# Kernel optimization log

Hardware: AMD Instinct MI355X
Metric: run time of the kernel (lower is better)

## Reference

```python
import jax, jax.numpy as jnp
import numpy as np

N_EMBD = 768
N_HEAD = 12
BLOCK_SIZE = 1024


def setup_inputs() -> dict:
    key = jax.random.key(0)
    ks = jax.random.split(key, 11)
    s = lambda fan_in: 1.0 / np.sqrt(fan_in)
    x = jax.random.normal(ks[0], (8, 1024, N_EMBD), dtype=jnp.float32)
    return {
        "x": x,
        "ln1_g": jnp.ones((N_EMBD,), jnp.float32),
        "ln1_b": jnp.zeros((N_EMBD,), jnp.float32),
        "w_attn": jax.random.normal(ks[1], (N_EMBD, 3 * N_EMBD), jnp.float32) * s(N_EMBD),
        "b_attn": jnp.zeros((3 * N_EMBD,), jnp.float32),
        "w_proj": jax.random.normal(ks[2], (N_EMBD, N_EMBD), jnp.float32) * s(N_EMBD),
        "b_proj": jnp.zeros((N_EMBD,), jnp.float32),
        "ln2_g": jnp.ones((N_EMBD,), jnp.float32),
        "ln2_b": jnp.zeros((N_EMBD,), jnp.float32),
        "w_fc": jax.random.normal(ks[3], (N_EMBD, 4 * N_EMBD), jnp.float32) * s(N_EMBD),
        "b_fc": jnp.zeros((4 * N_EMBD,), jnp.float32),
        "w_fc_proj": jax.random.normal(ks[4], (4 * N_EMBD, N_EMBD), jnp.float32) * s(4 * N_EMBD),
        "b_fc_proj": jnp.zeros((N_EMBD,), jnp.float32),
    }


def _layernorm(x, g, b, eps=1e-5):
    mu = jnp.mean(x, axis=-1, keepdims=True)
    var = jnp.var(x, axis=-1, keepdims=True)
    return (x - mu) * jax.lax.rsqrt(var + eps) * g + b


def _gelu_tanh(x):
    # GELU with tanh approximation (matches nn.GELU(approximate='tanh'))
    c = np.sqrt(2.0 / np.pi).astype(np.float32)
    return 0.5 * x * (1.0 + jnp.tanh(c * (x + 0.044715 * x * x * x)))


def _attn(x, w_attn, b_attn, w_proj, b_proj):
    B, T, C = x.shape
    hs = C // N_HEAD
    qkv = x @ w_attn + b_attn  # [B,T,3C]
    q, k, v = jnp.split(qkv, 3, axis=-1)
    # [B,T,C] -> [B,nh,T,hs]
    to_heads = lambda t: t.reshape(B, T, N_HEAD, hs).transpose(0, 2, 1, 3)
    q, k, v = to_heads(q), to_heads(k), to_heads(v)
    att = jnp.einsum('bhqd,bhkd->bhqk', q, k) * (1.0 / np.sqrt(hs))
    causal = jnp.tril(jnp.ones((T, T), bool))
    att = jnp.where(causal, att, -jnp.inf)
    att = jax.nn.softmax(att, axis=-1)
    y = jnp.einsum('bhqk,bhkd->bhqd', att, v)  # [B,nh,T,hs]
    y = y.transpose(0, 2, 1, 3).reshape(B, T, C)
    return y @ w_proj + b_proj


def reference(x, ln1_g, ln1_b, w_attn, b_attn, w_proj, b_proj,
              ln2_g, ln2_b, w_fc, b_fc, w_fc_proj, b_fc_proj):
    x = x + _attn(_layernorm(x, ln1_g, ln1_b), w_attn, b_attn, w_proj, b_proj)
    h = _layernorm(x, ln2_g, ln2_b)
    h = _gelu_tanh(h @ w_fc + b_fc) @ w_fc_proj + b_fc_proj
    return x + h
```

## Files before the change

kernel.cpp:

```cpp
#include <hip/hip_runtime.h>

typedef __bf16 bf16x8 __attribute__((ext_vector_type(8)));
typedef float  f32x4  __attribute__((ext_vector_type(4)));
typedef unsigned short ushort8 __attribute__((ext_vector_type(8)));

__device__ __forceinline__ unsigned short f2bf(float f) {
    unsigned u = __float_as_uint(f);
    u += 0x7FFFu + ((u >> 16) & 1u);
    return (unsigned short)(u >> 16);
}

__device__ __forceinline__ f32x4 mfma16x16x32(bf16x8 a, bf16x8 b, f32x4 c) {
    return __builtin_amdgcn_mfma_f32_16x16x32_bf16(a, b, c, 0, 0, 0);
}

__device__ __forceinline__ bf16x8 ld8(const unsigned short* p) {
    return __builtin_bit_cast(bf16x8, *(const ushort8*)p);
}

__device__ __forceinline__ float exp2_fast(float x) {
    float r; asm("v_exp_f32 %0, %1" : "=v"(r) : "v"(x)); return r;
}

__device__ __forceinline__ void glds16(const unsigned short* g, unsigned short* l) {
    __builtin_amdgcn_global_load_lds(
        (const __attribute__((address_space(1))) void*)g,
        (__attribute__((address_space(3))) void*)l, 16, 0, 0);
}

__device__ __forceinline__ float gelu_tanh(float x) {
    const float c = 0.7978845608028654f;
    float z = c * (x + 0.044715f * x * x * x);
    float e = __expf(2.f * z);
    float th = 1.f - 2.f / (e + 1.f);
    return 0.5f * x * (1.f + th);
}

#define N_EMBD 768
#define SEQ    1024
#define NHEAD  12
#define HS     64
#define MROWS  8192

__global__ __launch_bounds__(256) void tcast_kernel(const float* __restrict__ in,
                                                    unsigned short* __restrict__ out,
                                                    int K, int N) {
    __shared__ float tile[32][33];
    int nb = blockIdx.x * 32, kb = blockIdx.y * 32;
    int tx = threadIdx.x, ty = threadIdx.y;
#pragma unroll
    for (int i = 0; i < 4; i++) {
        int k = kb + ty + i * 8;
        tile[ty + i * 8][tx] = in[(size_t)k * N + nb + tx];
    }
    __syncthreads();
#pragma unroll
    for (int i = 0; i < 4; i++) {
        int n = nb + ty + i * 8;
        out[(size_t)n * K + kb + tx] = f2bf(tile[tx][ty + i * 8]);
    }
}

__global__ __launch_bounds__(256) void ln_kernel(const float* __restrict__ x,
                                                 const float* __restrict__ g,
                                                 const float* __restrict__ b,
                                                 unsigned short* __restrict__ out) {
    int row = blockIdx.x;
    const float* xr = x + (size_t)row * N_EMBD;
    float v[3], s = 0.f, s2 = 0.f;
#pragma unroll
    for (int i = 0; i < 3; i++) {
        v[i] = xr[threadIdx.x + i * 256];
        s += v[i]; s2 += v[i] * v[i];
    }
#pragma unroll
    for (int m = 1; m < 64; m <<= 1) { s += __shfl_xor(s, m); s2 += __shfl_xor(s2, m); }
    __shared__ float ps[4], ps2[4];
    int wid = threadIdx.x >> 6;
    if ((threadIdx.x & 63) == 0) { ps[wid] = s; ps2[wid] = s2; }
    __syncthreads();
    s  = ps[0] + ps[1] + ps[2] + ps[3];
    s2 = ps2[0] + ps2[1] + ps2[2] + ps2[3];
    float mu  = s * (1.f / N_EMBD);
    float var = s2 * (1.f / N_EMBD) - mu * mu;
    float inv = rsqrtf(var + 1e-5f);
#pragma unroll
    for (int i = 0; i < 3; i++) {
        int c = threadIdx.x + i * 256;
        out[(size_t)row * N_EMBD + c] = f2bf((v[i] - mu) * inv * g[c] + b[c]);
    }
}

template <int EPI, int WM>
__global__ __launch_bounds__(256) void gemm_bt_kernel(
    const unsigned short* __restrict__ A, const unsigned short* __restrict__ BT,
    const float* __restrict__ bias, const float* __restrict__ res,
    float* __restrict__ outF, unsigned short* __restrict__ outB,
    int M, int N, int K) {
    constexpr int BM = WM * 32;
    constexpr int ASZ = BM * 64;
    constexpr int BSZ = 128 * 64;
    __shared__ __attribute__((aligned(16))) unsigned short As[2 * ASZ];
    __shared__ __attribute__((aligned(16))) unsigned short Bs[2 * BSZ];
    const int gx = gridDim.x;
    const int slot = blockIdx.y * gx + blockIdx.x;
    const int chunk = (gx * gridDim.y) >> 3;
    const int logical = (slot & 7) * chunk + (slot >> 3);
    const int m0 = (logical / gx) * BM, n0 = (logical % gx) * 128;
    const int t = threadIdx.x, lane = t & 63, wid = t >> 6;
    const int wr = wid >> 1, wc = wid & 1;

    f32x4 acc[WM][4] = {};

    const int rrow = lane & 15, g = lane >> 4;
    const int swz8 = (rrow & 7) << 3;

    const int srow = t >> 3;
    const int scol = ((t & 7) ^ (srow & 7)) * 8;

    const int NT = K >> 6;
#pragma unroll
    for (int i = 0; i < WM; i++)
        glds16(&A[(size_t)(m0 + i * 32 + srow) * K + scol], &As[i * 2048 + wid * 512]);
#pragma unroll
    for (int i = 0; i < 4; i++)
        glds16(&BT[(size_t)(n0 + i * 32 + srow) * K + scol], &Bs[i * 2048 + wid * 512]);
    __syncthreads();

    int cur = 0;
    for (int kt = 0; kt < NT; ++kt) {
        if (kt + 1 < NT) {
            const int kk = (kt + 1) << 6;
            const int nb = (cur ^ 1);
#pragma unroll
            for (int i = 0; i < WM; i++)
                glds16(&A[(size_t)(m0 + i * 32 + srow) * K + kk + scol],
                       &As[nb * ASZ + i * 2048 + wid * 512]);
#pragma unroll
            for (int i = 0; i < 4; i++)
                glds16(&BT[(size_t)(n0 + i * 32 + srow) * K + kk + scol],
                       &Bs[nb * BSZ + i * 2048 + wid * 512]);
        }
        const unsigned short* ab = &As[cur * ASZ];
        const unsigned short* bb = &Bs[cur * BSZ];
#pragma unroll
        for (int s = 0; s < 2; s++) {
            bf16x8 af[WM], bfr[4];
#pragma unroll
            for (int i = 0; i < WM; i++) {
                int row = wr * (WM * 16) + i * 16 + rrow;
                af[i] = ld8(&ab[row * 64 + ((((s << 2) | g) << 3) ^ swz8)]);
            }
#pragma unroll
            for (int j = 0; j < 4; j++) {
                int row = wc * 64 + j * 16 + rrow;
                bfr[j] = ld8(&bb[row * 64 + ((((s << 2) | g) << 3) ^ swz8)]);
            }
#pragma unroll
            for (int i = 0; i < WM; i++)
#pragma unroll
                for (int j = 0; j < 4; j++) acc[i][j] = mfma16x16x32(af[i], bfr[j], acc[i][j]);
        }
        __syncthreads();
        cur ^= 1;
    }

    const int crow = g * 4, ccol = rrow;
#pragma unroll
    for (int i = 0; i < WM; i++) {
        int gr0 = m0 + wr * (WM * 16) + i * 16 + crow;
#pragma unroll
        for (int j = 0; j < 4; j++) {
            int gc = n0 + wc * 64 + j * 16 + ccol;
            float bv = bias[gc];
#pragma unroll
            for (int r = 0; r < 4; r++) {
                int gr = gr0 + r;
                float v = acc[i][j][r] + bv;
                if constexpr (EPI == 1) v = gelu_tanh(v);
                if constexpr (EPI == 2) {
                    outF[(size_t)gr * N + gc] = v + res[(size_t)gr * N + gc];
                } else {
                    outB[(size_t)gr * N + gc] = f2bf(v);
                }
            }
        }
    }
}

#define SCALE_LOG2E 0.18033688011112042f

__device__ __forceinline__ void attn_tile(
    const unsigned short* Ks, const unsigned short* Vt, unsigned short* P,
    const bf16x8* qf, f32x4* yacc, float* lrow,
    int q0w, int kv0, bool masked, int lane)
{
    const int rrow = lane & 15, g = lane >> 4, kg8 = g * 8;
    const int qrb = q0w + g * 4;
#pragma unroll
    for (int ct = 0; ct < 4; ct++) {
        const int j = ct * 16 + rrow;
        const unsigned short* kr = &Ks[j * 64];
        f32x4 z = {};
        z = mfma16x16x32(qf[0], ld8(&kr[((g    ) ^ (j & 7)) * 8]), z);
        z = mfma16x16x32(qf[1], ld8(&kr[((g + 4) ^ (j & 7)) * 8]), z);
        const int jj = kv0 + j;
#pragma unroll
        for (int r = 0; r < 4; r++) {
            float v = z[r] * SCALE_LOG2E;
            if (masked && jj > qrb + r) v = -1e30f;
            const int q = g * 4 + r;
            P[q * 80 + (j ^ ((q & 7) << 3))] = f2bf(exp2_fast(v));
        }
    }
    asm volatile("s_waitcnt lgkmcnt(0)" ::: "memory");
    __builtin_amdgcn_sched_barrier(0);
    const int sw = (rrow & 7) << 3;
    bf16x8 pa0 = ld8(&P[rrow * 80 + ((kg8     ) ^ sw)]);
    bf16x8 pa1 = ld8(&P[rrow * 80 + ((kg8 + 32) ^ sw)]);
    const bf16x8 vones = __builtin_bit_cast(bf16x8,
        (ushort8){0x3F80, 0x3F80, 0x3F80, 0x3F80, 0x3F80, 0x3F80, 0x3F80, 0x3F80});
    __builtin_amdgcn_s_setprio(1);
    f32x4 ss = {};
    ss = mfma16x16x32(pa0, vones, ss);
    ss = mfma16x16x32(pa1, vones, ss);
#pragma unroll
    for (int r = 0; r < 4; r++) lrow[r] += ss[r];
#pragma unroll
    for (int dt = 0; dt < 4; dt++) {
        const unsigned short* vr = &Vt[(dt * 16 + rrow) * 88];
        yacc[dt] = mfma16x16x32(pa0, ld8(&vr[kg8     ]), yacc[dt]);
        yacc[dt] = mfma16x16x32(pa1, ld8(&vr[kg8 + 32]), yacc[dt]);
    }
    __builtin_amdgcn_s_setprio(0);
}

__global__ __launch_bounds__(512, 6) void attn_kernel(const unsigned short* __restrict__ qkv,
                                                      unsigned short* __restrict__ yb) {
    const int slot = blockIdx.y * 8 + blockIdx.x;
    const int logical = (slot & 7) * 96 + (slot >> 3);
    const int p = logical & 7;
    const int bh = logical >> 3;
    const int b = bh / NHEAD, h = bh % NHEAD;
    const int t = threadIdx.x, lane = t & 63, wid = t >> 6;
    const int half = wid >> 2, w4 = wid & 3;
    const int qt = half ? p : (15 - p);
    const int ntSelf = half ? (p + 1) : (16 - p);
    const int ntMax = 16 - p;
    const int q0w = qt * 64 + w4 * 16;
    const int rrow = lane & 15, g = lane >> 4, kg8 = g * 8;

    __shared__ __attribute__((aligned(16))) unsigned short Ks[64 * 64];
    __shared__ __attribute__((aligned(16))) unsigned short Vt[64 * 88];
    __shared__ __attribute__((aligned(16))) unsigned short Ps[8][16 * 80];

    bf16x8 qf[2];
    {
        size_t base = ((size_t)(b * SEQ + q0w + rrow)) * 2304 + h * HS;
        qf[0] = ld8(&qkv[base + kg8]);
        qf[1] = ld8(&qkv[base + 32 + kg8]);
    }

    f32x4 y[4] = {};
    float lrow[4] = {0.f, 0.f, 0.f, 0.f};

    const int kr0 = t >> 3;
    const int kc0 = ((t & 7) ^ (kr0 & 7)) * 8;
    const int vd = t & 63, vk = (t >> 6) * 8;

    for (int tt = 0; tt < ntMax; tt++) {
        const int kv0 = tt * 64;
        __syncthreads();
        glds16(&qkv[((size_t)(b * SEQ + kv0 + kr0)) * 2304 + 768 + h * HS + kc0], &Ks[wid * 512]);
        ushort8 v8;
#pragma unroll
        for (int i = 0; i < 8; i++)
            v8[i] = qkv[((size_t)(b * SEQ + kv0 + vk + i)) * 2304 + 1536 + h * HS + vd];
        *(ushort8*)&Vt[vd * 88 + vk] = v8;
        __syncthreads();

        if (tt < ntSelf)
            attn_tile(Ks, Vt, &Ps[wid][0], qf, y, lrow, q0w, kv0, tt == ntSelf - 1, lane);
    }

#pragma unroll
    for (int dt = 0; dt < 4; dt++)
#pragma unroll
        for (int r = 0; r < 4; r++) {
            int col = h * HS + dt * 16 + rrow;
            yb[((size_t)(b * SEQ + q0w + g * 4 + r)) * N_EMBD + col] = f2bf(y[dt][r] / lrow[r]);
        }
}

extern "C" void kernel_launch(void* const* d_in, const int* in_sizes, int n_in,
                              void* d_out, int out_size, void* d_ws, size_t ws_size,
                              hipStream_t stream) {
    const float* x        = (const float*)d_in[0];
    const float* ln1_g    = (const float*)d_in[1];
    const float* ln1_b    = (const float*)d_in[2];
    const float* w_attn   = (const float*)d_in[3];
    const float* b_attn   = (const float*)d_in[4];
    const float* w_proj   = (const float*)d_in[5];
    const float* b_proj   = (const float*)d_in[6];
    const float* ln2_g    = (const float*)d_in[7];
    const float* ln2_b    = (const float*)d_in[8];
    const float* w_fc     = (const float*)d_in[9];
    const float* b_fc     = (const float*)d_in[10];
    const float* w_fcp    = (const float*)d_in[11];
    const float* b_fcp    = (const float*)d_in[12];
    float* out = (float*)d_out;

    unsigned short* ws = (unsigned short*)d_ws;
    unsigned short* wT_attn = ws;
    unsigned short* wT_proj = wT_attn + 2304 * 768;
    unsigned short* wT_fc   = wT_proj + 768 * 768;
    unsigned short* wT_fcp  = wT_fc   + 3072 * 768;
    unsigned short* xb      = wT_fcp  + 768 * 3072;
    unsigned short* qkv     = xb      + (size_t)MROWS * 768;
    unsigned short* yb      = qkv     + (size_t)MROWS * 2304;
    unsigned short* act     = qkv;
    float* x2 = (float*)(yb + (size_t)MROWS * 768);

    dim3 tb(32, 8);
    tcast_kernel<<<dim3(2304 / 32, 768 / 32), tb, 0, stream>>>(w_attn, wT_attn, 768, 2304);
    tcast_kernel<<<dim3(768 / 32, 768 / 32),  tb, 0, stream>>>(w_proj, wT_proj, 768, 768);
    tcast_kernel<<<dim3(3072 / 32, 768 / 32), tb, 0, stream>>>(w_fc,   wT_fc,   768, 3072);
    tcast_kernel<<<dim3(768 / 32, 3072 / 32), tb, 0, stream>>>(w_fcp,  wT_fcp,  3072, 768);

    ln_kernel<<<MROWS, 256, 0, stream>>>(x, ln1_g, ln1_b, xb);
    gemm_bt_kernel<0, 4><<<dim3(2304 / 128, MROWS / 128), 256, 0, stream>>>(
        xb, wT_attn, b_attn, nullptr, nullptr, qkv, MROWS, 2304, 768);
    attn_kernel<<<dim3(8, 96), 512, 0, stream>>>(qkv, yb);
    gemm_bt_kernel<2, 2><<<dim3(768 / 128, MROWS / 64), 256, 0, stream>>>(
        yb, wT_proj, b_proj, x, x2, nullptr, MROWS, 768, 768);
    ln_kernel<<<MROWS, 256, 0, stream>>>(x2, ln2_g, ln2_b, xb);
    gemm_bt_kernel<1, 4><<<dim3(3072 / 128, MROWS / 128), 256, 0, stream>>>(
        xb, wT_fc, b_fc, nullptr, nullptr, act, MROWS, 3072, 768);
    gemm_bt_kernel<2, 2><<<dim3(768 / 128, MROWS / 64), 256, 0, stream>>>(
        act, wT_fcp, b_fcp, x2, out, nullptr, MROWS, 768, 3072);
}
```

Before: 263.2 us.

## Triple-buffer GEMM K-loop with vmcnt-based waits and a single barrier per step

Expands the shared-memory A/B tiles from double to triple buffering and prefetches two K-tiles ahead. Each step waits with explicit s_waitcnt vmcnt counts, then a single s_barrier, replacing the trailing __syncthreads. This keeps more global-to-LDS loads in flight to hide memory latency. In exchange it uses more LDS per block, which may lower occupancy. The loop is unrolled by 3 and assumes NT is divisible by 3, which holds for K=768 and K=3072.

New measurement: 352.4 us. 33.9% more time.

```diff
diff --git a/kernel.cpp b/kernel.cpp
--- a/kernel.cpp
+++ b/kernel.cpp
@@ -100,8 +100,8 @@
     constexpr int BM = WM * 32;
     constexpr int ASZ = BM * 64;
     constexpr int BSZ = 128 * 64;
-    __shared__ __attribute__((aligned(16))) unsigned short As[2 * ASZ];
-    __shared__ __attribute__((aligned(16))) unsigned short Bs[2 * BSZ];
+    __shared__ __attribute__((aligned(16))) unsigned short As[3 * ASZ];
+    __shared__ __attribute__((aligned(16))) unsigned short Bs[3 * BSZ];
     const int gx = gridDim.x;
     const int slot = blockIdx.y * gx + blockIdx.x;
     const int chunk = (gx * gridDim.y) >> 3;
@@ -119,30 +119,32 @@
     const int scol = ((t & 7) ^ (srow & 7)) * 8;
 
     const int NT = K >> 6;
-#pragma unroll
-    for (int i = 0; i < WM; i++)
-        glds16(&A[(size_t)(m0 + i * 32 + srow) * K + scol], &As[i * 2048 + wid * 512]);
-#pragma unroll
-    for (int i = 0; i < 4; i++)
-        glds16(&BT[(size_t)(n0 + i * 32 + srow) * K + scol], &Bs[i * 2048 + wid * 512]);
-    __syncthreads();
-
-    int cur = 0;
-    for (int kt = 0; kt < NT; ++kt) {
-        if (kt + 1 < NT) {
-            const int kk = (kt + 1) << 6;
-            const int nb = (cur ^ 1);
-#pragma unroll
-            for (int i = 0; i < WM; i++)
-                glds16(&A[(size_t)(m0 + i * 32 + srow) * K + kk + scol],
-                       &As[nb * ASZ + i * 2048 + wid * 512]);
-#pragma unroll
-            for (int i = 0; i < 4; i++)
-                glds16(&BT[(size_t)(n0 + i * 32 + srow) * K + kk + scol],
-                       &Bs[nb * BSZ + i * 2048 + wid * 512]);
-        }
-        const unsigned short* ab = &As[cur * ASZ];
-        const unsigned short* bb = &Bs[cur * BSZ];
+
+    auto STAGE = [&](int kt, int buf) {
+        const int kk = kt << 6;
+#pragma unroll
+        for (int i = 0; i < WM; i++)
+            glds16(&A[(size_t)(m0 + i * 32 + srow) * K + kk + scol],
+                   &As[buf * ASZ + i * 2048 + wid * 512]);
+#pragma unroll
+        for (int i = 0; i < 4; i++)
+            glds16(&BT[(size_t)(n0 + i * 32 + srow) * K + kk + scol],
+                   &Bs[buf * BSZ + i * 2048 + wid * 512]);
+    };
+
+    auto ITER = [&](int kt, int buf, int sbuf) {
+        if (kt == NT - 1) {
+            asm volatile("s_waitcnt vmcnt(0)" ::: "memory");
+        } else if constexpr (WM == 4) {
+            asm volatile("s_waitcnt vmcnt(8)" ::: "memory");
+        } else {
+            asm volatile("s_waitcnt vmcnt(6)" ::: "memory");
+        }
+        __builtin_amdgcn_s_barrier();
+        __builtin_amdgcn_sched_barrier(0);
+        if (kt + 2 < NT) STAGE(kt + 2, sbuf);
+        const unsigned short* ab = &As[buf * ASZ];
+        const unsigned short* bb = &Bs[buf * BSZ];
 #pragma unroll
         for (int s = 0; s < 2; s++) {
             bf16x8 af[WM], bfr[4];
@@ -161,8 +163,14 @@
 #pragma unroll
                 for (int j = 0; j < 4; j++) acc[i][j] = mfma16x16x32(af[i], bfr[j], acc[i][j]);
         }
-        __syncthreads();
-        cur ^= 1;
+    };
+
+    STAGE(0, 0);
+    STAGE(1, 1);
+    for (int kt3 = 0; kt3 < NT; kt3 += 3) {
+        ITER(kt3,     0, 2);
+        ITER(kt3 + 1, 1, 0);
+        ITER(kt3 + 2, 2, 1);
     }
 
     const int crow = g * 4, ccol = rrow;
```

## Process both paired causal query tiles per wave to reuse K/V fragments

Applied to the files above, without the earlier changes.

The attention kernel drops from 512 to 256 threads per block. Each wave now handles two 16-row query strips, one from the early tile and one from the mirrored late tile, instead of eight waves each owning one strip. K and V fragments loaded from LDS are shared by both strips' MFMAs, which halves LDS fragment reads per MFMA and removes the idle waves that used to skip tiles. The cost is double the accumulator registers per wave, fewer waves per block, and each thread doing twice the K/V global-to-LDS staging.

New measurement: 260.0 us. No clear change (-1.2%).

```diff
diff --git a/kernel.cpp b/kernel.cpp
--- a/kernel.cpp
+++ b/kernel.cpp
@@ -190,52 +190,7 @@
 
 #define SCALE_LOG2E 0.18033688011112042f
 
-__device__ __forceinline__ void attn_tile(
-    const unsigned short* Ks, const unsigned short* Vt, unsigned short* P,
-    const bf16x8* qf, f32x4* yacc, float* lrow,
-    int q0w, int kv0, bool masked, int lane)
-{
-    const int rrow = lane & 15, g = lane >> 4, kg8 = g * 8;
-    const int qrb = q0w + g * 4;
-#pragma unroll
-    for (int ct = 0; ct < 4; ct++) {
-        const int j = ct * 16 + rrow;
-        const unsigned short* kr = &Ks[j * 64];
-        f32x4 z = {};
-        z = mfma16x16x32(qf[0], ld8(&kr[((g    ) ^ (j & 7)) * 8]), z);
-        z = mfma16x16x32(qf[1], ld8(&kr[((g + 4) ^ (j & 7)) * 8]), z);
-        const int jj = kv0 + j;
-#pragma unroll
-        for (int r = 0; r < 4; r++) {
-            float v = z[r] * SCALE_LOG2E;
-            if (masked && jj > qrb + r) v = -1e30f;
-            const int q = g * 4 + r;
-            P[q * 80 + (j ^ ((q & 7) << 3))] = f2bf(exp2_fast(v));
-        }
-    }
-    asm volatile("s_waitcnt lgkmcnt(0)" ::: "memory");
-    __builtin_amdgcn_sched_barrier(0);
-    const int sw = (rrow & 7) << 3;
-    bf16x8 pa0 = ld8(&P[rrow * 80 + ((kg8     ) ^ sw)]);
-    bf16x8 pa1 = ld8(&P[rrow * 80 + ((kg8 + 32) ^ sw)]);
-    const bf16x8 vones = __builtin_bit_cast(bf16x8,
-        (ushort8){0x3F80, 0x3F80, 0x3F80, 0x3F80, 0x3F80, 0x3F80, 0x3F80, 0x3F80});
-    __builtin_amdgcn_s_setprio(1);
-    f32x4 ss = {};
-    ss = mfma16x16x32(pa0, vones, ss);
-    ss = mfma16x16x32(pa1, vones, ss);
-#pragma unroll
-    for (int r = 0; r < 4; r++) lrow[r] += ss[r];
-#pragma unroll
-    for (int dt = 0; dt < 4; dt++) {
-        const unsigned short* vr = &Vt[(dt * 16 + rrow) * 88];
-        yacc[dt] = mfma16x16x32(pa0, ld8(&vr[kg8     ]), yacc[dt]);
-        yacc[dt] = mfma16x16x32(pa1, ld8(&vr[kg8 + 32]), yacc[dt]);
-    }
-    __builtin_amdgcn_s_setprio(0);
-}
-
-__global__ __launch_bounds__(512, 6) void attn_kernel(const unsigned short* __restrict__ qkv,
+__global__ __launch_bounds__(256, 4) void attn_kernel(const unsigned short* __restrict__ qkv,
                                                       unsigned short* __restrict__ yb) {
     const int slot = blockIdx.y * 8 + blockIdx.x;
     const int logical = (slot & 7) * 96 + (slot >> 3);
@@ -243,44 +198,133 @@
     const int bh = logical >> 3;
     const int b = bh / NHEAD, h = bh % NHEAD;
     const int t = threadIdx.x, lane = t & 63, wid = t >> 6;
-    const int half = wid >> 2, w4 = wid & 3;
-    const int qt = half ? p : (15 - p);
-    const int ntSelf = half ? (p + 1) : (16 - p);
-    const int ntMax = 16 - p;
-    const int q0w = qt * 64 + w4 * 16;
+    const int q0A = p * 64 + wid * 16, q0B = (15 - p) * 64 + wid * 16;
+    const int ntA = p + 1, ntB = 16 - p;
     const int rrow = lane & 15, g = lane >> 4, kg8 = g * 8;
 
     __shared__ __attribute__((aligned(16))) unsigned short Ks[64 * 64];
     __shared__ __attribute__((aligned(16))) unsigned short Vt[64 * 88];
-    __shared__ __attribute__((aligned(16))) unsigned short Ps[8][16 * 80];
-
-    bf16x8 qf[2];
+    __shared__ __attribute__((aligned(16))) unsigned short Ps[4][2][16 * 80];
+
+    bf16x8 qfA[2], qfB[2];
     {
-        size_t base = ((size_t)(b * SEQ + q0w + rrow)) * 2304 + h * HS;
-        qf[0] = ld8(&qkv[base + kg8]);
-        qf[1] = ld8(&qkv[base + 32 + kg8]);
-    }
-
-    f32x4 y[4] = {};
-    float lrow[4] = {0.f, 0.f, 0.f, 0.f};
-
-    const int kr0 = t >> 3;
+        size_t baseA = ((size_t)(b * SEQ + q0A + rrow)) * 2304 + h * HS;
+        qfA[0] = ld8(&qkv[baseA + kg8]);
+        qfA[1] = ld8(&qkv[baseA + 32 + kg8]);
+        size_t baseB = ((size_t)(b * SEQ + q0B + rrow)) * 2304 + h * HS;
+        qfB[0] = ld8(&qkv[baseB + kg8]);
+        qfB[1] = ld8(&qkv[baseB + 32 + kg8]);
+    }
+
+    f32x4 yA[4] = {}, yB[4] = {};
+    float lA[4] = {0.f, 0.f, 0.f, 0.f}, lB[4] = {0.f, 0.f, 0.f, 0.f};
+
+    const int kr0 = t >> 3, kr1 = kr0 + 32;
     const int kc0 = ((t & 7) ^ (kr0 & 7)) * 8;
-    const int vd = t & 63, vk = (t >> 6) * 8;
-
-    for (int tt = 0; tt < ntMax; tt++) {
+    const int vd = t & 63, vk = (t >> 6) * 16;
+
+    unsigned short* PB = &Ps[wid][0][0];
+    unsigned short* PA = &Ps[wid][1][0];
+    const bf16x8 vones = __builtin_bit_cast(bf16x8,
+        (ushort8){0x3F80, 0x3F80, 0x3F80, 0x3F80, 0x3F80, 0x3F80, 0x3F80, 0x3F80});
+
+    for (int tt = 0; tt < ntB; tt++) {
         const int kv0 = tt * 64;
+        const bool doA = (tt < ntA);
+        const bool maskB = (tt == ntB - 1), maskA = (tt == ntA - 1);
         __syncthreads();
         glds16(&qkv[((size_t)(b * SEQ + kv0 + kr0)) * 2304 + 768 + h * HS + kc0], &Ks[wid * 512]);
-        ushort8 v8;
+        glds16(&qkv[((size_t)(b * SEQ + kv0 + kr1)) * 2304 + 768 + h * HS + kc0], &Ks[2048 + wid * 512]);
+        ushort8 vlo, vhi;
 #pragma unroll
         for (int i = 0; i < 8; i++)
-            v8[i] = qkv[((size_t)(b * SEQ + kv0 + vk + i)) * 2304 + 1536 + h * HS + vd];
-        *(ushort8*)&Vt[vd * 88 + vk] = v8;
+            vlo[i] = qkv[((size_t)(b * SEQ + kv0 + vk + i)) * 2304 + 1536 + h * HS + vd];
+#pragma unroll
+        for (int i = 0; i < 8; i++)
+            vhi[i] = qkv[((size_t)(b * SEQ + kv0 + vk + 8 + i)) * 2304 + 1536 + h * HS + vd];
+        *(ushort8*)&Vt[vd * 88 + vk] = vlo;
+        *(ushort8*)&Vt[vd * 88 + vk + 8] = vhi;
         __syncthreads();
 
-        if (tt < ntSelf)
-            attn_tile(Ks, Vt, &Ps[wid][0], qf, y, lrow, q0w, kv0, tt == ntSelf - 1, lane);
+        f32x4 sB[4], sA[4];
+#pragma unroll
+        for (int ct = 0; ct < 4; ct++) {
+            const int j = ct * 16 + rrow;
+            const unsigned short* kr = &Ks[j * 64];
+            bf16x8 k0 = ld8(&kr[((g    ) ^ (j & 7)) * 8]);
+            bf16x8 k1 = ld8(&kr[((g + 4) ^ (j & 7)) * 8]);
+            f32x4 zB = {};
+            zB = mfma16x16x32(qfB[0], k0, zB);
+            zB = mfma16x16x32(qfB[1], k1, zB);
+            sB[ct] = zB;
+            if (doA) {
+                f32x4 zA = {};
+                zA = mfma16x16x32(qfA[0], k0, zA);
+                zA = mfma16x16x32(qfA[1], k1, zA);
+                sA[ct] = zA;
+            }
+        }
+        const int qrbB = q0B + g * 4, qrbA = q0A + g * 4;
+#pragma unroll
+        for (int ct = 0; ct < 4; ct++) {
+            const int j = ct * 16 + rrow, jj = kv0 + j;
+#pragma unroll
+            for (int r = 0; r < 4; r++) {
+                float v = sB[ct][r] * SCALE_LOG2E;
+                if (maskB && jj > qrbB + r) v = -1e30f;
+                const int q = g * 4 + r;
+                PB[q * 80 + (j ^ ((q & 7) << 3))] = f2bf(exp2_fast(v));
+            }
+        }
+        if (doA) {
+#pragma unroll
+            for (int ct = 0; ct < 4; ct++) {
+                const int j = ct * 16 + rrow, jj = kv0 + j;
+#pragma unroll
+                for (int r = 0; r < 4; r++) {
+                    float v = sA[ct][r] * SCALE_LOG2E;
+                    if (maskA && jj > qrbA + r) v = -1e30f;
+                    const int q = g * 4 + r;
+                    PA[q * 80 + (j ^ ((q & 7) << 3))] = f2bf(exp2_fast(v));
+                }
+            }
+        }
+        asm volatile("s_waitcnt lgkmcnt(0)" ::: "memory");
+        __builtin_amdgcn_sched_barrier(0);
+        const int sw = (rrow & 7) << 3;
+        bf16x8 paB0 = ld8(&PB[rrow * 80 + ((kg8     ) ^ sw)]);
+        bf16x8 paB1 = ld8(&PB[rrow * 80 + ((kg8 + 32) ^ sw)]);
+        bf16x8 paA0, paA1;
+        if (doA) {
+            paA0 = ld8(&PA[rrow * 80 + ((kg8     ) ^ sw)]);
+            paA1 = ld8(&PA[rrow * 80 + ((kg8 + 32) ^ sw)]);
+        }
+        __builtin_amdgcn_s_setprio(1);
+        f32x4 ssB = {};
+        ssB = mfma16x16x32(paB0, vones, ssB);
+        ssB = mfma16x16x32(paB1, vones, ssB);
+#pragma unroll
+        for (int r = 0; r < 4; r++) lB[r] += ssB[r];
+        if (doA) {
+            f32x4 ssA = {};
+            ssA = mfma16x16x32(paA0, vones, ssA);
+            ssA = mfma16x16x32(paA1, vones, ssA);
+#pragma unroll
+            for (int r = 0; r < 4; r++) lA[r] += ssA[r];
+        }
+#pragma unroll
+        for (int dt = 0; dt < 4; dt++) {
+            const unsigned short* vr = &Vt[(dt * 16 + rrow) * 88];
+            bf16x8 v0 = ld8(&vr[kg8]);
+            bf16x8 v1 = ld8(&vr[kg8 + 32]);
+            yB[dt] = mfma16x16x32(paB0, v0, yB[dt]);
+            yB[dt] = mfma16x16x32(paB1, v1, yB[dt]);
+            if (doA) {
+                yA[dt] = mfma16x16x32(paA0, v0, yA[dt]);
+                yA[dt] = mfma16x16x32(paA1, v1, yA[dt]);
+            }
+        }
+        __builtin_amdgcn_s_setprio(0);
     }
 
 #pragma unroll
@@ -288,7 +332,8 @@
 #pragma unroll
         for (int r = 0; r < 4; r++) {
             int col = h * HS + dt * 16 + rrow;
-            yb[((size_t)(b * SEQ + q0w + g * 4 + r)) * N_EMBD + col] = f2bf(y[dt][r] / lrow[r]);
+            yb[((size_t)(b * SEQ + q0B + g * 4 + r)) * N_EMBD + col] = f2bf(yB[dt][r] / lB[r]);
+            yb[((size_t)(b * SEQ + q0A + g * 4 + r)) * N_EMBD + col] = f2bf(yA[dt][r] / lA[r]);
         }
 }
 
@@ -330,7 +375,7 @@
     ln_kernel<<<MROWS, 256, 0, stream>>>(x, ln1_g, ln1_b, xb);
     gemm_bt_kernel<0, 4><<<dim3(2304 / 128, MROWS / 128), 256, 0, stream>>>(
         xb, wT_attn, b_attn, nullptr, nullptr, qkv, MROWS, 2304, 768);
-    attn_kernel<<<dim3(8, 96), 512, 0, stream>>>(qkv, yb);
+    attn_kernel<<<dim3(8, 96), 256, 0, stream>>>(qkv, yb);
     gemm_bt_kernel<2, 2><<<dim3(768 / 128, MROWS / 64), 256, 0, stream>>>(
         yb, wT_proj, b_proj, x, x2, nullptr, MROWS, 768, 768);
     ln_kernel<<<MROWS, 256, 0, stream>>>(x2, ln2_g, ln2_b, xb);
```
